# Performance work log

Hardware: AMD Instinct MI355X
Metric: run time of the kernel (lower is better)

The kernel has to match this reference:

```python
import jax, jax.numpy as jnp
import numpy as np

B, N, D, E, F, K = 2, 2048, 768, 8, 3072, 2
V_MAX = 3.0
FEAT_CLAMP = 10.0


def setup_inputs() -> dict:
    key = jax.random.key(0)
    ks = jax.random.split(key, 8)
    s = lambda k, shape, sc: (jax.random.normal(k, shape, jnp.float32) * sc)
    return {
        "x": s(ks[0], (B, N, D), 1.0),
        "v_w": s(ks[1], (D,), 0.02),
        "v_b": jnp.zeros((), jnp.float32),
        "gate_w": s(ks[2], (D, E), 0.02),
        "gate_b": jnp.zeros((E,), jnp.float32),
        "w1": s(ks[3], (E, D, F), 0.02),
        "b1": jnp.zeros((E, F), jnp.float32),
        "w2": s(ks[4], (E, F, D), 0.02),
        "b2": jnp.zeros((E, D), jnp.float32),
        "out_w": s(ks[5], (2, D), 0.02),
        "out_b": jnp.zeros((D,), jnp.float32),
        "bk_scale": jnp.ones((D,), jnp.float32),
    }


def bk_green_diag(a):
    # a: (B, N) complex64 diagonal of (H_eps - z), unit off-diagonals.
    # Stable two-sided continued-fraction (Thomas/LDU) recursion:
    #   d_i = a_i - 1/d_{i-1},  e_i = a_i - 1/e_{i+1},  G_ii = 1/(d_i + e_i - a_i)
    aT = jnp.swapaxes(a, 0, 1)  # (N, B)

    def step(c, ai):
        d = ai - 1.0 / c
        return d, d

    d0 = aT[0]
    _, d_rest = jax.lax.scan(step, d0, aT[1:])
    d = jnp.concatenate([d0[None], d_rest], axis=0)  # (N, B)

    eN = aT[-1]
    _, e_rest = jax.lax.scan(step, eN, aT[:-1], reverse=True)
    e = jnp.concatenate([e_rest, eN[None]], axis=0)  # (N, B)

    G = 1.0 / (d + e - aT)
    return jnp.swapaxes(G, 0, 1)  # (B, N) complex


def reference(x, v_w, v_b, gate_w, gate_b, w1, b1, w2, b2, out_w, out_b, bk_scale):
    # --- potential projection: v = clamp(Linear(x), +-3) ---
    v = jnp.clip(x @ v_w + v_b, -V_MAX, V_MAX)  # (B, N)
    # H_eps diagonal = -2 + v, z = 1j  ->  A = H_eps - z
    a = ((-2.0 + v).astype(jnp.complex64) - 1j)
    G = bk_green_diag(a)  # (B, N) complex
    feats = jnp.stack([G.real, G.imag], axis=-1)  # (B, N, 2)

    # --- sparse MoE FFN (top-k softmax gating, GELU experts) ---
    logits = x @ gate_w + gate_b  # (B, N, E)
    probs = jax.nn.softmax(logits, axis=-1)
    topv, topi = jax.lax.top_k(probs, K)
    topv = topv / jnp.sum(topv, axis=-1, keepdims=True)
    comb = jnp.sum(topv[..., None] * jax.nn.one_hot(topi, E, dtype=x.dtype), axis=2)  # (B, N, E)
    h = jax.nn.gelu(jnp.einsum("bnd,edf->bnef", x, w1) + b1)  # (B, N, E, F)
    y = jnp.einsum("bnef,efd->bned", h, w2) + b2  # (B, N, E, D)
    ffn_out = jnp.einsum("bne,bned->bnd", comb, y)

    # --- spectral branch: clamp features, project to d_model, scale ---
    feats_c = jnp.clip(feats, -FEAT_CLAMP, FEAT_CLAMP)
    spec_out = feats_c @ out_w + out_b  # (B, N, D)
    return ffn_out + bk_scale * spec_out
```

## Files before the change

### kernel.cpp

```cpp
#include <hip/hip_runtime.h>
#include <hip/hip_bf16.h>

#define BB 2
#define NN 2048
#define DD 768
#define EE 8
#define FF 3072
#define TOK (BB*NN)
#define ROWS_CAP 9216
#define TILES 72

typedef __attribute__((ext_vector_type(8))) __bf16 bf16x8;
typedef __attribute__((ext_vector_type(4))) float floatx4;

#define OFF_CTRL    0ull
#define OFF_V       1024ull
#define OFF_TOKE    17408ull
#define OFF_TOKW    50176ull
#define OFF_ROWTOK  82944ull
#define OFF_ROWW    119808ull
#define OFF_SLOT    156672ull
#define OFF_FEATS   189440ull
#define OFF_W2T     222208ull
#define OFF_XBF     37970944ull
#define OFF_W1T     44262400ull
#define OFF_H       82011136ull
#define OFF_Y       OFF_XBF

__device__ __forceinline__ ushort f2b(float f) {
    union { float f; unsigned int i; } v; v.f = f;
    unsigned int u = v.i;
    unsigned int r = (u + 0x7FFFu + ((u >> 16) & 1u)) >> 16;
    return (ushort)r;
}
__device__ __forceinline__ unsigned int pk2(float lo, float hi) {
    union { float f; unsigned int u; } a, b;
    a.f = lo; b.f = hi;
    unsigned int ra = ((a.u + 0x7FFFu + ((a.u >> 16) & 1u)) >> 16) & 0xFFFFu;
    unsigned int rb = (b.u + 0x7FFFu + ((b.u >> 16) & 1u)) & 0xFFFF0000u;
    return ra | rb;
}
__device__ __forceinline__ float gelu_f(float x) {
    float z = 0.7978845608028654f * x * (1.f + 0.044715f * x * x);
    z = fminf(fmaxf(z, -12.f), 12.f);
    float e = __expf(2.f * z);
    return 0.5f * x * (1.f + (e - 1.f) / (e + 1.f));
}
__device__ __forceinline__ void gload16(const ushort* g, ushort* l) {
    __builtin_amdgcn_global_load_lds((const __attribute__((address_space(1))) void*)g,
                                     (__attribute__((address_space(3))) void*)l,
                                     16, 0, 0);
}

struct cplx { float x, y; };
__device__ __forceinline__ cplx cmulc(cplx a, cplx b) { return {a.x*b.x - a.y*b.y, a.x*b.y + a.y*b.x}; }
__device__ __forceinline__ cplx caddc(cplx a, cplx b) { return {a.x + b.x, a.y + b.y}; }
__device__ __forceinline__ cplx cdivc(cplx a, cplx b) {
    float s = 1.f / (b.x*b.x + b.y*b.y);
    return {(a.x*b.x + a.y*b.y)*s, (a.y*b.x - a.x*b.y)*s};
}
struct mob { cplx m00, m01, m10, m11; };
__device__ __forceinline__ mob mmul(const mob& A, const mob& B) {
    mob C;
    C.m00 = caddc(cmulc(A.m00, B.m00), cmulc(A.m01, B.m10));
    C.m01 = caddc(cmulc(A.m00, B.m01), cmulc(A.m01, B.m11));
    C.m10 = caddc(cmulc(A.m10, B.m00), cmulc(A.m11, B.m10));
    C.m11 = caddc(cmulc(A.m10, B.m01), cmulc(A.m11, B.m11));
    return C;
}
__device__ __forceinline__ void mnorm(mob& A) {
    float s = fabsf(A.m00.x);
    s = fmaxf(s, fabsf(A.m00.y)); s = fmaxf(s, fabsf(A.m01.x)); s = fmaxf(s, fabsf(A.m01.y));
    s = fmaxf(s, fabsf(A.m10.x)); s = fmaxf(s, fabsf(A.m10.y)); s = fmaxf(s, fabsf(A.m11.x));
    s = fmaxf(s, fabsf(A.m11.y));
    float r = 1.f / fmaxf(s, 1e-30f);
    A.m00.x *= r; A.m00.y *= r; A.m01.x *= r; A.m01.y *= r;
    A.m10.x *= r; A.m10.y *= r; A.m11.x *= r; A.m11.y *= r;
}
__device__ __forceinline__ mob mstep(cplx a, const mob& P) {
    mob C;
    C.m00 = {a.x*P.m00.x - a.y*P.m00.y - P.m10.x, a.x*P.m00.y + a.y*P.m00.x - P.m10.y};
    C.m01 = {a.x*P.m01.x - a.y*P.m01.y - P.m11.x, a.x*P.m01.y + a.y*P.m01.x - P.m11.y};
    C.m10 = P.m00; C.m11 = P.m01;
    return C;
}
__device__ __forceinline__ void mstore(float* s, const mob& A) {
    s[0]=A.m00.x; s[1]=A.m00.y; s[2]=A.m01.x; s[3]=A.m01.y;
    s[4]=A.m10.x; s[5]=A.m10.y; s[6]=A.m11.x; s[7]=A.m11.y;
}
__device__ __forceinline__ mob mload(const float* s) {
    mob A;
    A.m00 = {s[0], s[1]}; A.m01 = {s[2], s[3]};
    A.m10 = {s[4], s[5]}; A.m11 = {s[6], s[7]};
    return A;
}

template<bool PERM>
__device__ __forceinline__ void tcvt64_body(
    const float* __restrict__ src, ushort* __restrict__ dst,
    int Rs, int Cs, int r0, int c0, ushort* __restrict__ tT , int tid)
{
    int lr = tid >> 2;
    int lc0 = (tid & 3) * 16;
    const float* sp = src + (size_t)(r0 + lr) * Cs + c0 + lc0;
    float4 v[4];
    #pragma unroll
    for (int u = 0; u < 4; u++) v[u] = *(const float4*)(sp + 4*u);
    int chw = lr >> 3, wbit = lr & 7;
    #pragma unroll
    for (int u = 0; u < 4; u++) {
        float vs[4] = {v[u].x, v[u].y, v[u].z, v[u].w};
        #pragma unroll
        for (int e2 = 0; e2 < 4; e2++) {
            int col = lc0 + 4*u + e2;
            int g = (col >> 4) & 3;
            tT[col * 72 + ((chw ^ g) << 3) + wbit] = f2b(vs[e2]);
        }
    }
    __syncthreads();
    int p = tid & 7;
    #pragma unroll
    for (int pass = 0; pass < 2; pass++) {
        int c = (tid >> 3) + pass * 32;
        int g = (c >> 4) & 3;
        int chl = p ^ g;
        int a64 = chl * 8;
        size_t off = (size_t)(c0 + c) * Rs + r0 + a64;
        if (PERM) {
            int g32 = (a64 >> 5) * 32;
            int a = a64 & 31;
            ushort o8[8] __attribute__((aligned(16)));
            #pragma unroll
            for (int k = 0; k < 8; k++) {
                int pk = a + k;
                int rl = g32 + (pk >> 1) + ((pk & 1) << 4);
                int phys = ((rl >> 3) ^ g) * 8 + (rl & 7);
                o8[k] = tT[c * 72 + phys];
            }
            *(uint4*)(dst + off) = *(const uint4*)o8;
        } else {
            *(uint4*)(dst + off) = *(const uint4*)(tT + c * 72 + p * 8);
        }
    }
}

#define NB_CVT   ((TOK*DD)/8/256)
#define NB_ROUTE (TOK/4)

__device__ __forceinline__ void cvt_body(const float* __restrict__ src, ushort* __restrict__ dst, int i) {
    const float4* s = ((const float4*)src) + (size_t)i * 2;
    float4 a = s[0], b = s[1];
    uint4 o;
    o.x = pk2(a.x, a.y); o.y = pk2(a.z, a.w);
    o.z = pk2(b.x, b.y); o.w = pk2(b.z, b.w);
    *(((uint4*)dst) + i) = o;
}

__device__ __forceinline__ void routing_body(
    const float* __restrict__ x, const float* __restrict__ v_w, const float* __restrict__ v_b,
    const float* __restrict__ gate_w, const float* __restrict__ gate_b,
    float* __restrict__ v_out, int* __restrict__ tok_e, float* __restrict__ tok_w, int blk)
{
    int wave = threadIdx.x >> 6, lane = threadIdx.x & 63;
    int t = blk * 4 + wave;
    const float* xr = x + (size_t)t * DD;
    float av = 0.f;
    float ag[8] = {0.f, 0.f, 0.f, 0.f, 0.f, 0.f, 0.f, 0.f};
    #pragma unroll
    for (int i = 0; i < 12; i++) {
        int d = lane + 64 * i;
        float xv = xr[d];
        av += xv * v_w[d];
        const float4* g = (const float4*)(gate_w + d * 8);
        float4 g0 = g[0], g1 = g[1];
        ag[0] += xv * g0.x; ag[1] += xv * g0.y; ag[2] += xv * g0.z; ag[3] += xv * g0.w;
        ag[4] += xv * g1.x; ag[5] += xv * g1.y; ag[6] += xv * g1.z; ag[7] += xv * g1.w;
    }
    #pragma unroll
    for (int off = 32; off >= 1; off >>= 1) {
        av += __shfl_xor(av, off);
        #pragma unroll
        for (int e = 0; e < 8; e++) ag[e] += __shfl_xor(ag[e], off);
    }
    if (lane == 0) {
        float vv = av + v_b[0];
        vv = fminf(fmaxf(vv, -3.f), 3.f);
        v_out[t] = vv;
        float lg[8];
        #pragma unroll
        for (int e = 0; e < 8; e++) lg[e] = ag[e] + gate_b[e];
        int e0 = 0;
        #pragma unroll
        for (int e = 1; e < 8; e++) if (lg[e] > lg[e0]) e0 = e;
        int e1 = -1;
        #pragma unroll
        for (int e = 0; e < 8; e++) if (e != e0 && (e1 < 0 || lg[e] > lg[e1])) e1 = e;
        float w0 = 1.f / (1.f + __expf(lg[e1] - lg[e0]));
        tok_e[2*t] = e0; tok_e[2*t+1] = e1;
        tok_w[2*t] = w0; tok_w[2*t+1] = 1.f - w0;
    }
}

__global__ __launch_bounds__(256) void prep0_kernel(
    const float* __restrict__ x, ushort* __restrict__ x_bf,
    const float* __restrict__ v_w, const float* __restrict__ v_b,
    const float* __restrict__ gate_w, const float* __restrict__ gate_b,
    float* __restrict__ v_out, int* __restrict__ tok_e, float* __restrict__ tok_w)
{
    int id = blockIdx.x;
    if (id < NB_CVT) { cvt_body(x, x_bf, id * 256 + threadIdx.x); return; }
    id -= NB_CVT;
    routing_body(x, v_w, v_b, gate_w, gate_b, v_out, tok_e, tok_w, id);
}

#define NB_W1T4  (12*48*EE/4)

__device__ void setup_body(
    const int* __restrict__ tok_e, const float* __restrict__ tok_w,
    int* __restrict__ ctrl, int* __restrict__ row_token, float* __restrict__ row_w,
    int* __restrict__ slot)
{
    __shared__ int cnt[8], base[8], cursor[8];
    int tid = threadIdx.x;
    int lane = tid & 63;
    if (tid < 8) { cnt[tid] = 0; cursor[tid] = 0; }
    __syncthreads();

    int mye[8];
    #pragma unroll
    for (int it = 0; it < 8; it++) {
        int idx = it * 1024 + tid;
        int e = tok_e[idx];
        mye[it] = e;
        #pragma unroll
        for (int ex = 0; ex < 8; ex++) {
            unsigned long long m = __ballot(e == ex);
            if (e == ex && lane == (__ffsll((long long)m) - 1))
                atomicAdd(&cnt[ex], (int)__popcll(m));
        }
    }
    __syncthreads();
    if (tid == 0) {
        int b = 0;
        int* te = ctrl + 24;
        for (int i = 0; i < TILES; i++) te[i] = -1;
        #pragma unroll
        for (int e = 0; e < EE; e++) {
            base[e] = b;
            ctrl[16 + e] = b;
            int tiles = (cnt[e] + 127) >> 7;
            int t0 = b >> 7;
            for (int i = 0; i < tiles; i++) te[t0 + i] = e;
            b += tiles << 7;
        }
    }
    for (int p = tid; p < ROWS_CAP; p += 1024) row_token[p] = -1;
    __syncthreads();

    #pragma unroll
    for (int it = 0; it < 8; it++) {
        int idx = it * 1024 + tid;
        int e = mye[it];
        unsigned long long lt = (1ull << lane) - 1ull;
        int p = 0;
        #pragma unroll
        for (int ex = 0; ex < 8; ex++) {
            unsigned long long m = __ballot(e == ex);
            if (e == ex) {
                int leader = __ffsll((long long)m) - 1;
                int pos = (int)__popcll(m & lt);
                int bp = 0;
                if (lane == leader) bp = atomicAdd(&cursor[ex], (int)__popcll(m));
                bp = __shfl(bp, leader);
                p = base[ex] + bp + pos;
            }
        }
        row_token[p] = idx >> 1;
        row_w[p] = tok_w[idx];
        slot[idx] = p;
    }
}

__device__ void bk_body(int b, const float* __restrict__ v, float* __restrict__ feats) {
    int t = threadIdx.x;
    bool act = t < 256;
    __shared__ float sm[256][8];
    const mob I = {{1.f,0.f},{0.f,0.f},{0.f,0.f},{1.f,0.f}};
    cplx a[8];
    const float* vb = v + (size_t)b * NN;
    if (act) {
        #pragma unroll
        for (int j = 0; j < 8; j++) { a[j].x = -2.f + vb[t*8 + j]; a[j].y = -1.f; }
    }

    mob cur = I;
    if (act) {
        #pragma unroll
        for (int j = 0; j < 8; j++) cur = mstep(a[j], cur);
        mnorm(cur);
        mstore(sm[t], cur);
    }
    for (int s = 1; s < 256; s <<= 1) {
        __syncthreads();
        mob prev; bool has = act && (t >= s);
        if (has) prev = mload(sm[t - s]);
        __syncthreads();
        if (has) { cur = mmul(cur, prev); mnorm(cur); mstore(sm[t], cur); }
    }
    __syncthreads();
    cplx dreg[8];
    if (act) {
        mob P = (t > 0) ? mload(sm[t - 1]) : I;
        #pragma unroll
        for (int j = 0; j < 8; j++) {
            P = mstep(a[j], P); mnorm(P);
            dreg[j] = cdivc(P.m00, P.m10);
        }
    }
    __syncthreads();

    cur = I;
    if (act) {
        #pragma unroll
        for (int j = 7; j >= 0; j--) cur = mstep(a[j], cur);
        mnorm(cur);
        mstore(sm[t], cur);
    }
    for (int s = 1; s < 256; s <<= 1) {
        __syncthreads();
        mob nxt; bool has = act && (t + s < 256);
        if (has) nxt = mload(sm[t + s]);
        __syncthreads();
        if (has) { cur = mmul(cur, nxt); mnorm(cur); mstore(sm[t], cur); }
    }
    __syncthreads();
    if (act) {
        mob P = (t < 255) ? mload(sm[t + 1]) : I;
        #pragma unroll
        for (int j = 7; j >= 0; j--) {
            P = mstep(a[j], P); mnorm(P);
            cplx e = cdivc(P.m00, P.m10);
            cplx den = {dreg[j].x + e.x - a[j].x, dreg[j].y + e.y - a[j].y};
            cplx one = {1.f, 0.f};
            cplx G = cdivc(one, den);
            int i = b * NN + t*8 + j;
            feats[2*i]   = G.x;
            feats[2*i+1] = G.y;
        }
    }
}

__global__ __launch_bounds__(1024) void setup_bk_kernel(
    const int* __restrict__ tok_e, const float* __restrict__ tok_w,
    int* __restrict__ ctrl, int* __restrict__ row_token, float* __restrict__ row_w,
    int* __restrict__ slot, const float* __restrict__ v, float* __restrict__ feats,
    const float* __restrict__ w1, ushort* __restrict__ w1t)
{
    if (blockIdx.x == 0) { setup_body(tok_e, tok_w, ctrl, row_token, row_w, slot); return; }
    if (blockIdx.x <= BB) { bk_body(blockIdx.x - 1, v, feats); return; }
    __shared__ __align__(16) ushort tT4[4 * 4608];
    int tt = (blockIdx.x - 1 - BB) * 4 + (threadIdx.x >> 8);
    int e = tt / (12 * 48);
    int rem = tt - e * 12 * 48;
    int cy = rem / 12;
    int rx = rem - cy * 12;
    tcvt64_body<false>(w1 + (size_t)e * DD * FF, w1t + (size_t)e * FF * DD,
                       DD, FF, rx * 64, cy * 64,
                       tT4 + (threadIdx.x >> 8) * 4608, threadIdx.x & 255);
}

#define MFMAS() do { \
        _Pragma("unroll") \
        for (int i = 0; i < 4; i++) \
            _Pragma("unroll") \
            for (int j = 0; j < 4; j++) \
                acc[i][j] = __builtin_amdgcn_mfma_f32_16x16x32_bf16(afr[i], bfr[j], acc[i][j], 0, 0, 0); \
    } while (0)

#define G1N   (24 * 36)
#define NW2T  (48 * 12 * EE / 2)

__global__ __launch_bounds__(512, 4) void gemm1_fused_kernel(
    const ushort* __restrict__ x_bf, const ushort* __restrict__ w1t, const float* __restrict__ b1,
    const int* __restrict__ ctrl, const int* __restrict__ row_token, ushort* __restrict__ H,
    const float* __restrict__ w2, ushort* __restrict__ w2t)
{
    __shared__ __align__(16) ushort SH[4][256 * 32];
    __shared__ int toks[256];
    int bid = blockIdx.x;
    int tid = threadIdx.x;

    if (bid >= G1N) {
        int tt = (bid - G1N) * 2 + (tid >> 8);
        int e = tt / (48 * 12);
        int rem = tt - e * 48 * 12;
        int cy = rem / 48;
        int rx = rem - cy * 48;
        ushort* tT = &SH[0][0] + (tid >> 8) * 4608;
        tcvt64_body<true>(w2 + (size_t)e * FF * DD, w2t + (size_t)e * DD * FF,
                          FF, DD, rx * 64, cy * 64, tT, tid & 255);
        return;
    }

    int fx = bid % 24;
    int tile = bid / 24;
    int e0 = ctrl[24 + 2*tile];
    if (e0 < 0) return;
    int e1 = ctrl[24 + 2*tile + 1];
    if (e1 < 0) e1 = e0;
    int p0 = tile * 256;
    int f0 = fx * 128;

    ushort* As0 = &SH[0][0];
    ushort* As1 = &SH[1][0];
    ushort* Bs0 = &SH[2][0];
    ushort* Bs1 = &SH[3][0];

    if (tid < 256) { int tk = row_token[p0 + tid]; toks[tid] = tk < 0 ? 0 : tk; }
    __syncthreads();

    int wave = tid >> 6, lane = tid & 63;
    int rsub = lane >> 2;
    int kq = (((lane & 3) ^ ((rsub >> 1) & 3))) * 8;
    int tokA0 = toks[wave*32 + rsub];
    int tokA1 = toks[wave*32 + 16 + rsub];
    const ushort* aglob0 = x_bf + (size_t)tokA0 * DD + kq;
    const ushort* aglob1 = x_bf + (size_t)tokA1 * DD + kq;
    int eh = (wave >> 2) ? e1 : e0;
    const ushort* w1e = w1t + (size_t)eh * (FF * DD);
    const ushort* bglob0 = w1e + (size_t)(f0 + (wave & 3)*32 + rsub) * DD + kq;
    const ushort* bglob1 = bglob0 + (size_t)16 * DD;
    ushort* AsW0 = As0 + wave * 32 * 32;
    ushort* BsW0 = Bs0 + wave * 32 * 32;
    ushort* AsW1 = As1 + wave * 32 * 32;
    ushort* BsW1 = Bs1 + wave * 32 * 32;

    floatx4 zero4 = {0.f, 0.f, 0.f, 0.f};
    floatx4 acc[4][4];
    #pragma unroll
    for (int i = 0; i < 4; i++)
        #pragma unroll
        for (int j = 0; j < 4; j++) acc[i][j] = zero4;

    int wm = (wave >> 1) * 64, wn = (wave & 1) * 64;
    int bbase = (wave >> 2) * 128;
    int lm = lane & 15, q = lane >> 4;
    int qx = (q ^ ((lm >> 1) & 3)) * 8;

    #define G1_STAGE(AW, BW, k0) do { \
        gload16(aglob0 + (k0), (AW)); \
        gload16(aglob1 + (k0), (AW) + 16*32); \
        gload16(bglob0 + (k0), (BW)); \
        gload16(bglob1 + (k0), (BW) + 16*32); } while (0)

    G1_STAGE(AsW0, BsW0, 0);
    G1_STAGE(AsW1, BsW1, 32);
    const int NK = DD / 32;
    for (int ks = 0; ks < NK; ks++) {
        int cur = ks & 1;
        const ushort* Ab = cur ? As1 : As0;
        const ushort* Bb = cur ? Bs1 : Bs0;
        ushort* AsN = cur ? AsW1 : AsW0;
        ushort* BsN = cur ? BsW1 : BsW0;
        if (ks < NK - 1) { asm volatile("s_waitcnt vmcnt(4)" ::: "memory"); }
        else             { asm volatile("s_waitcnt vmcnt(0)" ::: "memory"); }
        __builtin_amdgcn_s_barrier();
        bf16x8 afr[4], bfr[4];
        #pragma unroll
        for (int i = 0; i < 4; i++)
            afr[i] = *(const bf16x8*)(const void*)(Ab + (wm + i*16 + lm) * 32 + qx);
        #pragma unroll
        for (int j = 0; j < 4; j++)
            bfr[j] = *(const bf16x8*)(const void*)(Bb + (bbase + wn + j*16 + lm) * 32 + qx);
        asm volatile("s_waitcnt lgkmcnt(0)" ::: "memory");
        __builtin_amdgcn_sched_barrier(0);
        __builtin_amdgcn_s_barrier();
        if (ks + 2 < NK) G1_STAGE(AsN, BsN, ks*32 + 64);
        __builtin_amdgcn_s_setprio(1);
        MFMAS();
        __builtin_amdgcn_s_setprio(0);
    }
    #undef G1_STAGE

    #pragma unroll
    for (int i = 0; i < 4; i++) {
        #pragma unroll
        for (int jp = 0; jp < 2; jp++) {
            float bias0 = b1[eh * FF + f0 + wn + (2*jp)*16 + lm];
            float bias1 = b1[eh * FF + f0 + wn + (2*jp+1)*16 + lm];
            #pragma unroll
            for (int r = 0; r < 4; r++) {
                int m = wm + i*16 + q*4 + r;
                float h0 = gelu_f(acc[i][2*jp][r] + bias0);
                float h1 = gelu_f(acc[i][2*jp+1][r] + bias1);
                *(unsigned int*)(H + (size_t)(p0 + m) * FF + f0 + wn + jp*32 + lm*2) = pk2(h0, h1);
            }
        }
    }
}

#define STAGE64(AW, BW, k0) do { \
        _Pragma("unroll") \
        for (int g = 0; g < 4; g++) { \
            gload16(ag[g] + (k0), (AW) + g*8*64); \
            gload16(bg[g] + (k0), (BW) + g*8*64); \
        } } while (0)

#define LOADFR64(APTR, BPTR, QX) do { \
        _Pragma("unroll") \
        for (int i = 0; i < 4; i++) \
            afr[i] = *(const bf16x8*)(const void*)((APTR) + (wm + i*16 + lm) * 64 + (QX)); \
        _Pragma("unroll") \
        for (int j = 0; j < 4; j++) \
            bfr[j] = *(const bf16x8*)(const void*)((BPTR) + (wn + j*16 + lm) * 64 + (QX)); \
    } while (0)

#define PIPE64(NK) do { \
    STAGE64(AsW0, BsW0, 0); \
    STAGE64(AsW1, BsW1, 64); \
    for (int ks = 0; ks < (NK); ks++) { \
        int cur = ks & 1; \
        const ushort* Ab = cur ? As[1] : As[0]; \
        const ushort* Bb = cur ? Bs[1] : Bs[0]; \
        ushort* AsN = cur ? AsW1 : AsW0; \
        ushort* BsN = cur ? BsW1 : BsW0; \
        if (ks < (NK) - 1) { asm volatile("s_waitcnt vmcnt(8)" ::: "memory"); } \
        else               { asm volatile("s_waitcnt vmcnt(0)" ::: "memory"); } \
        __builtin_amdgcn_s_barrier(); \
        { \
            bf16x8 afr[4], bfr[4]; \
            LOADFR64(Ab, Bb, qx0); \
            __builtin_amdgcn_s_setprio(1); \
            MFMAS(); \
            __builtin_amdgcn_s_setprio(0); \
        } \
        { \
            bf16x8 afr[4], bfr[4]; \
            LOADFR64(Ab, Bb, qx0 ^ 32); \
            asm volatile("s_waitcnt lgkmcnt(0)" ::: "memory"); \
            __builtin_amdgcn_sched_barrier(0); \
            __builtin_amdgcn_s_barrier(); \
            if (ks + 2 < (NK)) STAGE64(AsN, BsN, ks*64 + 128); \
            __builtin_amdgcn_s_setprio(1); \
            MFMAS(); \
            __builtin_amdgcn_s_setprio(0); \
        } \
    } } while (0)

__global__ __launch_bounds__(256) void gemm2_kernel(
    const ushort* __restrict__ H, const ushort* __restrict__ w2t, const float* __restrict__ b2,
    const int* __restrict__ ctrl, const float* __restrict__ row_w, float* __restrict__ Y)
{
    int tile = blockIdx.x;
    int e = ctrl[24 + tile];
    if (e < 0) return;
    int p0 = tile * 128;
    int d0 = blockIdx.y * 128;

    __shared__ ushort As[2][128 * 64];
    __shared__ ushort Bs[2][128 * 64];

    int tid = threadIdx.x;
    int wave = tid >> 6, lane = tid & 63;
    int srow = lane >> 3;
    int kq = (((lane & 7) ^ (srow & 7))) * 8;
    const ushort* ag[4];
    #pragma unroll
    for (int g = 0; g < 4; g++)
        ag[g] = H + (size_t)(p0 + wave*32 + g*8 + srow) * FF + kq;
    const ushort* w2e = w2t + (size_t)e * (DD * FF);
    const ushort* bg[4];
    #pragma unroll
    for (int g = 0; g < 4; g++)
        bg[g] = w2e + (size_t)(d0 + wave*32 + g*8 + srow) * FF + kq;
    ushort* AsW0 = &As[0][wave * 32 * 64];
    ushort* BsW0 = &Bs[0][wave * 32 * 64];
    ushort* AsW1 = &As[1][wave * 32 * 64];
    ushort* BsW1 = &Bs[1][wave * 32 * 64];

    floatx4 zero4 = {0.f, 0.f, 0.f, 0.f};
    floatx4 acc[4][4];
    #pragma unroll
    for (int i = 0; i < 4; i++)
        #pragma unroll
        for (int j = 0; j < 4; j++) acc[i][j] = zero4;

    int wm = (wave & 1) * 64, wn = (wave >> 1) * 64;
    int lm = lane & 15, q = lane >> 4;
    int qx0 = (q ^ (lm & 7)) * 8;

    PIPE64(FF/64);

    #pragma unroll
    for (int i = 0; i < 4; i++) {
        #pragma unroll
        for (int j = 0; j < 4; j++) {
            int n = wn + j*16 + lm;
            float bias = b2[e * DD + d0 + n];
            #pragma unroll
            for (int r = 0; r < 4; r++) {
                int m = wm + i*16 + q*4 + r;
                float wgt = row_w[p0 + m];
                Y[(size_t)(p0 + m) * DD + d0 + n] = wgt * (acc[i][j][r] + bias);
            }
        }
    }
}

__global__ __launch_bounds__(256) void final_kernel(
    const float* __restrict__ Y, const int* __restrict__ slot, const float* __restrict__ feats,
    const float* __restrict__ out_w, const float* __restrict__ out_b,
    const float* __restrict__ bk_scale, float* __restrict__ out)
{
    int idx = blockIdx.x * 256 + threadIdx.x;
    int base = idx * 4;
    int t = base / DD;
    int d = base - t * DD;
    int p0 = slot[2*t], p1 = slot[2*t + 1];
    const float4 ya = *(const float4*)(Y + (size_t)p0 * DD + d);
    const float4 yb = *(const float4*)(Y + (size_t)p1 * DD + d);
    float f0 = feats[2*t], f1 = feats[2*t + 1];
    f0 = fminf(fmaxf(f0, -10.f), 10.f);
    f1 = fminf(fmaxf(f1, -10.f), 10.f);
    float ff[4] = {ya.x + yb.x, ya.y + yb.y, ya.z + yb.z, ya.w + yb.w};
    float4 o;
    float* op = (float*)&o;
    #pragma unroll
    for (int u = 0; u < 4; u++) {
        float spec = f0 * out_w[d + u] + f1 * out_w[DD + d + u] + out_b[d + u];
        op[u] = ff[u] + bk_scale[d + u] * spec;
    }
    *(float4*)(out + base) = o;
}

extern "C" void kernel_launch(void* const* d_in, const int* in_sizes, int n_in,
                              void* d_out, int out_size, void* d_ws, size_t ws_size,
                              hipStream_t stream)
{
    const float* x      = (const float*)d_in[0];
    const float* v_w    = (const float*)d_in[1];
    const float* v_b    = (const float*)d_in[2];
    const float* gate_w = (const float*)d_in[3];
    const float* gate_b = (const float*)d_in[4];
    const float* w1     = (const float*)d_in[5];
    const float* b1     = (const float*)d_in[6];
    const float* w2     = (const float*)d_in[7];
    const float* b2     = (const float*)d_in[8];
    const float* out_w  = (const float*)d_in[9];
    const float* out_b  = (const float*)d_in[10];
    const float* bk_s   = (const float*)d_in[11];

    char* ws = (char*)d_ws;
    int*    ctrl    = (int*)(ws + OFF_CTRL);
    float*  v       = (float*)(ws + OFF_V);
    int*    tok_e   = (int*)(ws + OFF_TOKE);
    float*  tok_w   = (float*)(ws + OFF_TOKW);
    int*    row_tok = (int*)(ws + OFF_ROWTOK);
    float*  row_w   = (float*)(ws + OFF_ROWW);
    int*    slot    = (int*)(ws + OFF_SLOT);
    float*  feats   = (float*)(ws + OFF_FEATS);
    ushort* w2t     = (ushort*)(ws + OFF_W2T);
    ushort* x_bf    = (ushort*)(ws + OFF_XBF);
    ushort* w1t     = (ushort*)(ws + OFF_W1T);
    ushort* H       = (ushort*)(ws + OFF_H);
    float*  Y       = (float*)(ws + OFF_Y);
    float*  out     = (float*)d_out;

    prep0_kernel<<<NB_CVT + NB_ROUTE, 256, 0, stream>>>(
        x, x_bf, v_w, v_b, gate_w, gate_b, v, tok_e, tok_w);
    setup_bk_kernel<<<1 + BB + NB_W1T4, 1024, 0, stream>>>(
        tok_e, tok_w, ctrl, row_tok, row_w, slot, v, feats, w1, w1t);
    gemm1_fused_kernel<<<G1N + NW2T, 512, 0, stream>>>(x_bf, w1t, b1, ctrl, row_tok, H, w2, w2t);
    gemm2_kernel<<<dim3(TILES, DD / 128), 256, 0, stream>>>(H, w2t, b2, ctrl, row_w, Y);
    final_kernel<<<(TOK * DD) / 1024, 256, 0, stream>>>(Y, slot, feats, out_w, out_b, bk_s, out);
}
```

Baseline: 186.5 us.

## Retile expert GEMM1 to 128x256 tiles with K=64 triple-buffered pipeline

Reworks the first expert GEMM so each block handles 128 routed rows of a single expert against 256 output features, instead of 256 rows spanning two experts against 128 features. The K step grows from 32 to 64 and uses a three-slot LDS ring with an 8-way XOR swizzle. Block indices are remapped so neighbouring blocks share feature tiles. The aim is more reuse per load and fewer barriers per K step, at the cost of a larger LDS footprint and launch bounds cut from 4 to 2 blocks per CU, which lowers occupancy.

```diff
diff --git a/kernel.cpp b/kernel.cpp
--- a/kernel.cpp
+++ b/kernel.cpp
@@ -377,16 +377,16 @@
                 acc[i][j] = __builtin_amdgcn_mfma_f32_16x16x32_bf16(afr[i], bfr[j], acc[i][j], 0, 0, 0); \
     } while (0)
 
-#define G1N   (24 * 36)
+#define G1N   (72 * 12)
 #define NW2T  (48 * 12 * EE / 2)
 
-__global__ __launch_bounds__(512, 4) void gemm1_fused_kernel(
+__global__ __launch_bounds__(512, 2) void gemm1_fused_kernel(
     const ushort* __restrict__ x_bf, const ushort* __restrict__ w1t, const float* __restrict__ b1,
     const int* __restrict__ ctrl, const int* __restrict__ row_token, ushort* __restrict__ H,
     const float* __restrict__ w2, ushort* __restrict__ w2t)
 {
-    __shared__ __align__(16) ushort SH[4][256 * 32];
-    __shared__ int toks[256];
+    __shared__ __align__(16) ushort SH[73728];
+    __shared__ int toks[128];
     int bid = blockIdx.x;
     int tid = threadIdx.x;
 
@@ -396,44 +396,48 @@
         int rem = tt - e * 48 * 12;
         int cy = rem / 48;
         int rx = rem - cy * 48;
-        ushort* tT = &SH[0][0] + (tid >> 8) * 4608;
+        ushort* tT = SH + (tid >> 8) * 4608;
         tcvt64_body<true>(w2 + (size_t)e * FF * DD, w2t + (size_t)e * DD * FF,
                           FF, DD, rx * 64, cy * 64, tT, tid & 255);
         return;
     }
 
-    int fx = bid % 24;
-    int tile = bid / 24;
-    int e0 = ctrl[24 + 2*tile];
-    if (e0 < 0) return;
-    int e1 = ctrl[24 + 2*tile + 1];
-    if (e1 < 0) e1 = e0;
-    int p0 = tile * 256;
-    int f0 = fx * 128;
-
-    ushort* As0 = &SH[0][0];
-    ushort* As1 = &SH[1][0];
-    ushort* Bs0 = &SH[2][0];
-    ushort* Bs1 = &SH[3][0];
-
-    if (tid < 256) { int tk = row_token[p0 + tid]; toks[tid] = tk < 0 ? 0 : tk; }
+    int x = bid & 7, s = bid >> 3;
+    int fx = s / 9;
+    int tile = x * 9 + (s - fx * 9);
+    int e = ctrl[24 + tile];
+    if (e < 0) return;
+    int p0 = tile * 128;
+    int f0 = fx * 256;
+
+    ushort* B3 = SH + 3 * 8192;
+
+    if (tid < 128) { int tk = row_token[p0 + tid]; toks[tid] = tk < 0 ? 0 : tk; }
     __syncthreads();
 
     int wave = tid >> 6, lane = tid & 63;
-    int rsub = lane >> 2;
-    int kq = (((lane & 3) ^ ((rsub >> 1) & 3))) * 8;
-    int tokA0 = toks[wave*32 + rsub];
-    int tokA1 = toks[wave*32 + 16 + rsub];
-    const ushort* aglob0 = x_bf + (size_t)tokA0 * DD + kq;
-    const ushort* aglob1 = x_bf + (size_t)tokA1 * DD + kq;
-    int eh = (wave >> 2) ? e1 : e0;
-    const ushort* w1e = w1t + (size_t)eh * (FF * DD);
-    const ushort* bglob0 = w1e + (size_t)(f0 + (wave & 3)*32 + rsub) * DD + kq;
-    const ushort* bglob1 = bglob0 + (size_t)16 * DD;
-    ushort* AsW0 = As0 + wave * 32 * 32;
-    ushort* BsW0 = Bs0 + wave * 32 * 32;
-    ushort* AsW1 = As1 + wave * 32 * 32;
-    ushort* BsW1 = Bs1 + wave * 32 * 32;
+    int wr = wave >> 2, wc = wave & 3;
+    int w16 = wave * 16;
+
+    int srow = lane >> 3;
+    int kq = ((lane & 7) ^ srow) * 8;
+    int tokA0 = toks[w16 + srow];
+    int tokA1 = toks[w16 + 8 + srow];
+    const ushort* aA0 = x_bf + (size_t)tokA0 * DD + kq;
+    const ushort* aA1 = x_bf + (size_t)tokA1 * DD + kq;
+    const ushort* w1e = w1t + (size_t)e * (FF * DD);
+    const ushort* bB00 = w1e + (size_t)(f0 +       w16 + srow) * DD + kq;
+    const ushort* bB01 = w1e + (size_t)(f0 +       w16 + 8 + srow) * DD + kq;
+    const ushort* bB10 = w1e + (size_t)(f0 + 128 + w16 + srow) * DD + kq;
+    const ushort* bB11 = w1e + (size_t)(f0 + 128 + w16 + 8 + srow) * DD + kq;
+    int dA0 = w16 * 64;
+    int dA1 = dA0 + 512;
+
+    int lm = lane & 15, q = lane >> 4;
+    int qa0 = ((q    ) ^ (lm & 7)) * 8;
+    int qa1 = ((q | 4) ^ (lm & 7)) * 8;
+    int arow = (wr * 64 + lm) * 64;
+    int brow = (wc * 64 + lm) * 64;
 
     floatx4 zero4 = {0.f, 0.f, 0.f, 0.f};
     floatx4 acc[4][4];
@@ -442,58 +446,67 @@
         #pragma unroll
         for (int j = 0; j < 4; j++) acc[i][j] = zero4;
 
-    int wm = (wave >> 1) * 64, wn = (wave & 1) * 64;
-    int bbase = (wave >> 2) * 128;
-    int lm = lane & 15, q = lane >> 4;
-    int qx = (q ^ ((lm >> 1) & 3)) * 8;
-
-    #define G1_STAGE(AW, BW, k0) do { \
-        gload16(aglob0 + (k0), (AW)); \
-        gload16(aglob1 + (k0), (AW) + 16*32); \
-        gload16(bglob0 + (k0), (BW)); \
-        gload16(bglob1 + (k0), (BW) + 16*32); } while (0)
-
-    G1_STAGE(AsW0, BsW0, 0);
-    G1_STAGE(AsW1, BsW1, 32);
-    const int NK = DD / 32;
-    for (int ks = 0; ks < NK; ks++) {
-        int cur = ks & 1;
-        const ushort* Ab = cur ? As1 : As0;
-        const ushort* Bb = cur ? Bs1 : Bs0;
-        ushort* AsN = cur ? AsW1 : AsW0;
-        ushort* BsN = cur ? BsW1 : BsW0;
-        if (ks < NK - 1) { asm volatile("s_waitcnt vmcnt(4)" ::: "memory"); }
-        else             { asm volatile("s_waitcnt vmcnt(0)" ::: "memory"); }
-        __builtin_amdgcn_s_barrier();
-        bf16x8 afr[4], bfr[4];
-        #pragma unroll
-        for (int i = 0; i < 4; i++)
-            afr[i] = *(const bf16x8*)(const void*)(Ab + (wm + i*16 + lm) * 32 + qx);
-        #pragma unroll
-        for (int j = 0; j < 4; j++)
-            bfr[j] = *(const bf16x8*)(const void*)(Bb + (bbase + wn + j*16 + lm) * 32 + qx);
-        asm volatile("s_waitcnt lgkmcnt(0)" ::: "memory");
-        __builtin_amdgcn_sched_barrier(0);
-        __builtin_amdgcn_s_barrier();
-        if (ks + 2 < NK) G1_STAGE(AsN, BsN, ks*32 + 64);
-        __builtin_amdgcn_s_setprio(1);
-        MFMAS();
-        __builtin_amdgcn_s_setprio(0);
-    }
-    #undef G1_STAGE
+    #define STG_A(SL, kt) do { \
+        gload16(aA0 + (kt)*64, SH + (SL)*8192 + dA0); \
+        gload16(aA1 + (kt)*64, SH + (SL)*8192 + dA1); } while (0)
+    #define STG_B(SL, kt) do { \
+        gload16(bB00 + (kt)*64, B3 + (SL)*16384 + dA0); \
+        gload16(bB01 + (kt)*64, B3 + (SL)*16384 + dA1); \
+        gload16(bB10 + (kt)*64, B3 + (SL)*16384 + 8192 + dA0); \
+        gload16(bB11 + (kt)*64, B3 + (SL)*16384 + 8192 + dA1); } while (0)
+
+    #define G1_PHASE(SL, QH) do { \
+        bf16x8 afr[4], bfr[4]; \
+        _Pragma("unroll") \
+        for (int i = 0; i < 4; i++) \
+            afr[i] = *(const bf16x8*)(const void*)(SH + (SL)*8192 + arow + i*1024 + (QH)); \
+        _Pragma("unroll") \
+        for (int j = 0; j < 4; j++) \
+            bfr[j] = *(const bf16x8*)(const void*)(B3 + (SL)*16384 + brow + j*1024 + (QH)); \
+        asm volatile("s_waitcnt lgkmcnt(0)" ::: "memory"); \
+        __builtin_amdgcn_sched_barrier(0); \
+        __builtin_amdgcn_s_setprio(1); \
+        MFMAS(); \
+        __builtin_amdgcn_s_setprio(0); } while (0)
+
+    #define G1_TILE(kt, SL, S2) do { \
+        bool st_ = (kt) < 10; \
+        if (st_) STG_A(S2, (kt) + 2); \
+        G1_PHASE(SL, qa0); \
+        __builtin_amdgcn_s_barrier(); \
+        if (st_) STG_B(S2, (kt) + 2); \
+        G1_PHASE(SL, qa1); \
+        if (st_)            { asm volatile("s_waitcnt vmcnt(6)" ::: "memory"); } \
+        else if ((kt) < 11) { asm volatile("s_waitcnt vmcnt(0)" ::: "memory"); } \
+        __builtin_amdgcn_s_barrier(); } while (0)
+
+    STG_A(0, 0); STG_B(0, 0);
+    STG_A(1, 1); STG_B(1, 1);
+    asm volatile("s_waitcnt vmcnt(6)" ::: "memory");
+    __builtin_amdgcn_s_barrier();
+
+    for (int kb = 0; kb < 12; kb += 3) {
+        G1_TILE(kb    , 0, 2);
+        G1_TILE(kb + 1, 1, 0);
+        G1_TILE(kb + 2, 2, 1);
+    }
+    #undef G1_TILE
+    #undef G1_PHASE
+    #undef STG_B
+    #undef STG_A
 
     #pragma unroll
     for (int i = 0; i < 4; i++) {
         #pragma unroll
         for (int jp = 0; jp < 2; jp++) {
-            float bias0 = b1[eh * FF + f0 + wn + (2*jp)*16 + lm];
-            float bias1 = b1[eh * FF + f0 + wn + (2*jp+1)*16 + lm];
+            float bias0 = b1[e * FF + f0 + wc*64 + (2*jp)*16 + lm];
+            float bias1 = b1[e * FF + f0 + wc*64 + (2*jp+1)*16 + lm];
             #pragma unroll
             for (int r = 0; r < 4; r++) {
-                int m = wm + i*16 + q*4 + r;
+                int m = wr*64 + i*16 + q*4 + r;
                 float h0 = gelu_f(acc[i][2*jp][r] + bias0);
                 float h1 = gelu_f(acc[i][2*jp+1][r] + bias1);
-                *(unsigned int*)(H + (size_t)(p0 + m) * FF + f0 + wn + jp*32 + lm*2) = pk2(h0, h1);
+                *(unsigned int*)(H + (size_t)(p0 + m) * FF + f0 + wc*64 + jp*32 + lm*2) = pk2(h0, h1);
             }
         }
     }
```

Result: slower. 208.1 us (+11.6%).
